# Optimization experiments

Measured on AMD Instinct MI355X. Metric: run time of the kernel, lower is better.

The kernel has to match this reference:

```python
import jax, jax.numpy as jnp
import numpy as np

N_NODES = 50000
N_EDGES = 800000
D_IN = 512
D_OUT = 256


def setup_inputs() -> dict:
    key = jax.random.key(0)
    k1, k2, k3 = jax.random.split(key, 3)
    x = jax.random.normal(k1, (N_NODES, D_IN), dtype=jnp.float32)
    edge_index = jax.random.randint(k2, (2, N_EDGES), 0, N_NODES, dtype=jnp.int64)
    # Glorot-style init for the GCN weight, zero bias (PyG defaults)
    W = jax.random.normal(k3, (D_IN, D_OUT), dtype=jnp.float32) * (1.0 / np.sqrt(D_IN))
    b = jnp.zeros((D_OUT,), dtype=jnp.float32)
    return {"x": x, "edge_index": edge_index, "W": W, "b": b}


def reference(x, edge_index, W, b):
    N = x.shape[0]
    # 1) dense linear transform (the compute-heavy GEMM)
    xw = x @ W  # [N, d_out]

    # 2) add self-loops (PyG GCNConv default)
    loop = jnp.arange(N, dtype=edge_index.dtype)
    row = jnp.concatenate([edge_index[0], loop])  # sources
    col = jnp.concatenate([edge_index[1], loop])  # targets

    # 3) symmetric normalization deg^{-1/2} on targets (in-degree incl. self-loops)
    deg = jax.ops.segment_sum(jnp.ones_like(col, dtype=xw.dtype), col, num_segments=N)
    dinv = jnp.where(deg > 0, jax.lax.rsqrt(deg), 0.0)
    norm = dinv[row] * dinv[col]  # [E+N]

    # 4) gather source features, scale, scatter-add to targets
    msgs = xw[row] * norm[:, None]  # [E+N, d_out]
    agg = jax.ops.segment_sum(msgs, col, num_segments=N)  # [N, d_out]

    # 5) bias + ReLU (dropout is identity in eval mode)
    return jax.nn.relu(agg + b)
```

## Files before the change

kernel.cpp:

```cpp
#include <hip/hip_runtime.h>
#include <hip/hip_bf16.h>

#define N_NODES 50000
#define N_EDGES 800000
#define D_IN    512
#define D_OUT   256
#define NBLK_SCAN ((N_NODES + 1023) / 1024)
#define GEMM_NWG (((N_NODES + 127) / 128) * 2)
#define GEMM_Q   (GEMM_NWG / 8)
#define GEMM_R   (GEMM_NWG % 8)

typedef short s8v  __attribute__((ext_vector_type(8)));
typedef float f32x4 __attribute__((ext_vector_type(4)));

__device__ __forceinline__ unsigned short bf16b(float f) {
    __hip_bfloat16 h = __float2bfloat16(f);
    return *reinterpret_cast<unsigned short*>(&h);
}
__device__ __forceinline__ float bflo(unsigned u) { return __uint_as_float(u << 16); }
__device__ __forceinline__ float bfhi(unsigned u) { return __uint_as_float(u & 0xffff0000u); }

#define GLD16(gp, lp)                                                           \
    __builtin_amdgcn_global_load_lds(                                           \
        (const __attribute__((address_space(1))) unsigned int*)(const void*)(gp),\
        (__attribute__((address_space(3))) unsigned int*)(void*)(lp), 16, 0, 0)

__device__ __forceinline__ int wave_incl_scan(int v, int lane) {
    #pragma unroll
    for (int d = 1; d < 64; d <<= 1) {
        int u = __shfl_up(v, d, 64);
        if (lane >= d) v += u;
    }
    return v;
}


__global__ void k_count(const int* __restrict__ col, int* __restrict__ cnt) {
    int i = (blockIdx.x * 256 + threadIdx.x) * 2;
    if (i < N_EDGES) {
        int2 c = *(const int2*)&col[i];
        atomicAdd(&cnt[c.x], 1);
        atomicAdd(&cnt[c.y], 1);
    }
}

__launch_bounds__(256)
__global__ void k_scan1(const int* __restrict__ cnt, int* __restrict__ bsum) {
    const int t = threadIdx.x, b = blockIdx.x;
    const int idx = b * 1024 + t * 4;
    int4 v = make_int4(0, 0, 0, 0);
    if (idx < N_NODES) v = *(const int4*)&cnt[idx];
    int s = v.x + v.y + v.z + v.w;
    #pragma unroll
    for (int d = 1; d < 64; d <<= 1) s += __shfl_xor(s, d, 64);
    __shared__ int ws[4];
    if ((t & 63) == 0) ws[t >> 6] = s;
    __syncthreads();
    if (t == 0) bsum[b] = ws[0] + ws[1] + ws[2] + ws[3];
}

__launch_bounds__(256)
__global__ void k_scan3(const int* __restrict__ cnt, const int* __restrict__ bsum,
                        int* __restrict__ row_ptr, float* __restrict__ dinv,
                        int* __restrict__ cursor) {
    const int t = threadIdx.x, b = blockIdx.x;
    const int lane = t & 63, wv = t >> 6;
    const int idx = b * 1024 + t * 4;
    int4 v = make_int4(0, 0, 0, 0);
    if (idx < N_NODES) v = *(const int4*)&cnt[idx];
    int s = v.x + v.y + v.z + v.w;
    int isc = wave_incl_scan(s, lane);
    __shared__ int wsum[4];
    __shared__ int s_boff;
    if (lane == 63) wsum[wv] = isc;
    if (t < 64) {
        int u = (t < b) ? bsum[t] : 0;
        #pragma unroll
        for (int d = 1; d < 64; d <<= 1) u += __shfl_xor(u, d, 64);
        if (t == 0) s_boff = u;
    }
    __syncthreads();
    int off = s_boff;
    #pragma unroll
    for (int i = 0; i < 4; ++i)
        if (i < wv) off += wsum[i];
    int p0 = off + isc - s;
    int p1 = p0 + v.x;
    int p2 = p1 + v.y;
    int p3 = p2 + v.z;
    if (idx < N_NODES) {
        row_ptr[idx + 0] = p0; cursor[idx + 0] = p0; dinv[idx + 0] = rsqrtf(1.f + (float)v.x);
        row_ptr[idx + 1] = p1; cursor[idx + 1] = p1; dinv[idx + 1] = rsqrtf(1.f + (float)v.y);
        row_ptr[idx + 2] = p2; cursor[idx + 2] = p2; dinv[idx + 2] = rsqrtf(1.f + (float)v.z);
        row_ptr[idx + 3] = p3; cursor[idx + 3] = p3; dinv[idx + 3] = rsqrtf(1.f + (float)v.w);
    }
    if (b == 0 && t == 0) row_ptr[N_NODES] = N_EDGES;
}

__global__ void k_fill(const int* __restrict__ row, const int* __restrict__ col,
                       int* __restrict__ cursor, int* __restrict__ csr_src) {
    int i = (blockIdx.x * 256 + threadIdx.x) * 2;
    if (i < N_EDGES) {
        int2 c = *(const int2*)&col[i];
        int2 r = *(const int2*)&row[i];
        int p0 = atomicAdd(&cursor[c.x], 1);
        csr_src[p0] = r.x;
        int p1 = atomicAdd(&cursor[c.y], 1);
        csr_src[p1] = r.y;
    }
}

__global__ void k_wt(const float* __restrict__ W, unsigned short* __restrict__ Wt) {
    int k = blockIdx.x;
    int n = threadIdx.x;
    Wt[(size_t)n * D_IN + k] = bf16b(W[(size_t)k * D_OUT + n]);
}

__launch_bounds__(256)
__global__ void k_gemm(const float* __restrict__ A,
                       const unsigned short* __restrict__ Wt,
                       const float* __restrict__ dinv,
                       unsigned short* __restrict__ yb)
{
    __shared__ __align__(16) float          As[128 * 32];
    __shared__ __align__(16) unsigned short Bs[128 * 32];

    int orig = blockIdx.x;
    int xcd = orig % 8, pos = orig / 8;
    int wg = (xcd < GEMM_R) ? xcd * (GEMM_Q + 1) + pos
                            : GEMM_R * (GEMM_Q + 1) + (xcd - GEMM_R) * GEMM_Q + pos;
    const int nt = wg & 1;
    const int mt = wg >> 1;
    const int m0 = mt * 128;
    const int n0 = nt * 128;

    const int t  = threadIdx.x;
    const int w  = t >> 6;
    const int l  = t & 63;
    const int wm = (w >> 1) * 64;
    const int wn = (w & 1) * 64;
    const int lr = l & 15;
    const int lk = l >> 4;

    size_t aoff[4];
    #pragma unroll
    for (int i = 0; i < 4; ++i) {
        int r = m0 + w * 32 + i * 8 + (l >> 3);
        if (r >= N_NODES) r = 0;
        aoff[i] = (size_t)r * D_IN + ((l & 7) ^ (l >> 3)) * 4;
    }
    size_t boff[2];
    #pragma unroll
    for (int i = 0; i < 2; ++i) {
        int r = n0 + w * 32 + i * 16 + (l >> 2);
        boff[i] = (size_t)r * D_IN + ((l & 3) ^ ((l >> 3) & 3)) * 8;
    }

    f32x4 acc[4][4] = {};

    #pragma unroll 1
    for (int tk = 0; tk < 16; ++tk) {
        const int kk = tk * 32;
        {
            char* ab = (char*)As + w * 4096;
            char* bb = (char*)Bs + w * 2048;
            #pragma unroll
            for (int i = 0; i < 4; ++i) GLD16(&A[aoff[i] + kk], ab + i * 1024);
            #pragma unroll
            for (int i = 0; i < 2; ++i) GLD16(&Wt[boff[i] + kk], bb + i * 1024);
        }
        __syncthreads();
        {
            s8v af[4], bfr[4];
            #pragma unroll
            for (int f = 0; f < 4; ++f) {
                int row = wm + f * 16 + lr;
                int s0  = (2 * lk) ^ (lr & 7);
                const char* pr = (const char*)As + row * 128;
                float4 x0 = *(const float4*)(pr + s0 * 16);
                float4 x1 = *(const float4*)(pr + (s0 ^ 1) * 16);
                union { s8v v; unsigned short h[8]; } u;
                u.h[0] = bf16b(x0.x); u.h[1] = bf16b(x0.y);
                u.h[2] = bf16b(x0.z); u.h[3] = bf16b(x0.w);
                u.h[4] = bf16b(x1.x); u.h[5] = bf16b(x1.y);
                u.h[6] = bf16b(x1.z); u.h[7] = bf16b(x1.w);
                af[f] = u.v;
            }
            #pragma unroll
            for (int f = 0; f < 4; ++f) {
                int row = wn + f * 16 + lr;
                int s   = lk ^ ((lr >> 1) & 3);
                bfr[f] = *(const s8v*)((const char*)Bs + row * 64 + s * 16);
            }
            #pragma unroll
            for (int fm = 0; fm < 4; ++fm)
                #pragma unroll
                for (int fn = 0; fn < 4; ++fn)
                    acc[fm][fn] = __builtin_amdgcn_mfma_f32_16x16x32_bf16(
                        af[fm], bfr[fn], acc[fm][fn], 0, 0, 0);
        }
        __syncthreads();
    }

    #pragma unroll
    for (int fm = 0; fm < 4; ++fm) {
        #pragma unroll
        for (int j = 0; j < 4; ++j) {
            int row = m0 + wm + fm * 16 + lk * 4 + j;
            if (row < N_NODES) {
                float s = dinv[row];
                #pragma unroll
                for (int fn = 0; fn < 4; ++fn) {
                    int col = n0 + wn + fn * 16 + lr;
                    yb[(size_t)row * D_OUT + col] = bf16b(acc[fm][fn][j] * s);
                }
            }
        }
    }
}

__device__ __forceinline__ void add8(float* acc, uint4 q) {
    unsigned x;
    x = q.x; acc[0] += bflo(x); acc[1] += bfhi(x);
    x = q.y; acc[2] += bflo(x); acc[3] += bfhi(x);
    x = q.z; acc[4] += bflo(x); acc[5] += bfhi(x);
    x = q.w; acc[6] += bflo(x); acc[7] += bfhi(x);
}

__launch_bounds__(256)
__global__ void k_gather(const int* __restrict__ row_ptr, const int* __restrict__ csr_src,
                         const unsigned short* __restrict__ yb, const float* __restrict__ dinv,
                         const float* __restrict__ bias, float* __restrict__ out)
{
    const int c  = blockIdx.x * 4 + (threadIdx.x >> 6);
    const int l  = threadIdx.x & 63;
    const int eg = l >> 5;
    const int cs = l & 31;
    const size_t colb = (size_t)cs * 8;

    float acc[8] = {0.f,0.f,0.f,0.f,0.f,0.f,0.f,0.f};

    const int s = row_ptr[c];
    const int e = row_ptr[c + 1];

    int i = s + eg;
    while (i + 14 < e) {
        int r[8];
        #pragma unroll
        for (int u = 0; u < 8; ++u) r[u] = csr_src[i + 2 * u];
        uint4 v[8];
        #pragma unroll
        for (int u = 0; u < 8; ++u) v[u] = *(const uint4*)&yb[(size_t)r[u] * D_OUT + colb];
        #pragma unroll
        for (int u = 0; u < 8; ++u) add8(acc, v[u]);
        i += 16;
    }
    while (i < e) {
        int r[4];
        #pragma unroll
        for (int u = 0; u < 4; ++u) {
            int p = i + 2 * u;
            r[u] = csr_src[p < e ? p : e - 1];
        }
        uint4 v[4];
        #pragma unroll
        for (int u = 0; u < 4; ++u) v[u] = *(const uint4*)&yb[(size_t)r[u] * D_OUT + colb];
        #pragma unroll
        for (int u = 0; u < 4; ++u)
            if (i + 2 * u < e) add8(acc, v[u]);
        i += 8;
    }

    #pragma unroll
    for (int u = 0; u < 8; ++u) acc[u] += __shfl_xor(acc[u], 32, 64);

    uint4 sv = *(const uint4*)&yb[(size_t)c * D_OUT + colb];
    add8(acc, sv);

    if (eg == 0) {
        const float sc = dinv[c];
        float4 b0 = *(const float4*)&bias[colb];
        float4 b1 = *(const float4*)&bias[colb + 4];
        float4 o0, o1;
        o0.x = fmaxf(fmaf(acc[0], sc, b0.x), 0.f);
        o0.y = fmaxf(fmaf(acc[1], sc, b0.y), 0.f);
        o0.z = fmaxf(fmaf(acc[2], sc, b0.z), 0.f);
        o0.w = fmaxf(fmaf(acc[3], sc, b0.w), 0.f);
        o1.x = fmaxf(fmaf(acc[4], sc, b1.x), 0.f);
        o1.y = fmaxf(fmaf(acc[5], sc, b1.y), 0.f);
        o1.z = fmaxf(fmaf(acc[6], sc, b1.z), 0.f);
        o1.w = fmaxf(fmaf(acc[7], sc, b1.w), 0.f);
        float* dst = &out[(size_t)c * D_OUT + colb];
        *(float4*)dst       = o0;
        *(float4*)(dst + 4) = o1;
    }
}

extern "C" void kernel_launch(void* const* d_in, const int* in_sizes, int n_in,
                              void* d_out, int out_size, void* d_ws, size_t ws_size,
                              hipStream_t stream) {
    const float* x   = (const float*)d_in[0];
    const int*   ei  = (const int*)d_in[1];
    const float* W   = (const float*)d_in[2];
    const float* b   = (const float*)d_in[3];
    float*       out = (float*)d_out;

    const int* row = ei;
    const int* col = ei + N_EDGES;

    char* p = (char*)d_ws;
    unsigned short* yb = (unsigned short*)p;  p += (size_t)N_NODES * D_OUT * 2;
    unsigned short* Wt = (unsigned short*)p;  p += (size_t)D_OUT * D_IN * 2;
    int*   csr_src = (int*)p;                 p += (size_t)N_EDGES * 4;
    int*   cnt     = (int*)p;                 p += (size_t)N_NODES * 4;
    int*   row_ptr = (int*)p;                 p += (size_t)(N_NODES + 4) * 4;
    int*   cursor  = (int*)p;                 p += (size_t)N_NODES * 4;
    float* dinv    = (float*)p;               p += (size_t)N_NODES * 4;
    int*   bsum    = (int*)p;                 p += (size_t)NBLK_SCAN * 4;

    hipMemsetAsync(cnt, 0, (size_t)N_NODES * sizeof(int), stream);
    k_count<<<(N_EDGES / 2 + 255) / 256, 256, 0, stream>>>(col, cnt);
    k_scan1<<<NBLK_SCAN, 256, 0, stream>>>(cnt, bsum);
    k_scan3<<<NBLK_SCAN, 256, 0, stream>>>(cnt, bsum, row_ptr, dinv, cursor);
    k_fill <<<(N_EDGES / 2 + 255) / 256, 256, 0, stream>>>(row, col, cursor, csr_src);
    k_wt   <<<D_IN, D_OUT, 0, stream>>>(W, Wt);

    k_gemm<<<GEMM_NWG, 256, 0, stream>>>(x, Wt, dinv, yb);

    k_gather<<<N_NODES / 4, 256, 0, stream>>>(row_ptr, csr_src, yb, dinv, b, out);
}
```

Before: 209.2 us.

## Retile GEMM to single-wave 64x64 blocks with 32x32 MFMA; fold memset into k_wt

The GEMM moves from 256-thread 128x128 workgroups using 16x16x32 MFMAs to single-wave 64x64 workgroups using 32x32x16 bf16 MFMAs. Blocks are remapped to XCDs with a simple strided mapping, and offsets use 32-bit arithmetic. Separately, the hipMemsetAsync of the degree counts is folded into the weight-transpose kernel, which now runs first, saving one launch. Smaller tiles give more workgroups and fewer cross-wave barriers, but each tile gets less operand reuse and A is re-read four times across the N tiles.

After: 217.0 us. 1.04x slower.

```diff
diff --git a/kernel.cpp b/kernel.cpp
--- a/kernel.cpp
+++ b/kernel.cpp
@@ -6,12 +6,11 @@
 #define D_IN    512
 #define D_OUT   256
 #define NBLK_SCAN ((N_NODES + 1023) / 1024)
-#define GEMM_NWG (((N_NODES + 127) / 128) * 2)
-#define GEMM_Q   (GEMM_NWG / 8)
-#define GEMM_R   (GEMM_NWG % 8)
-
-typedef short s8v  __attribute__((ext_vector_type(8)));
-typedef float f32x4 __attribute__((ext_vector_type(4)));
+#define GEMM_NWG (((N_NODES + 63) / 64) * 4)
+#define GEMM_CPX (GEMM_NWG / 8)
+
+typedef short s8v   __attribute__((ext_vector_type(8)));
+typedef float f32x16 __attribute__((ext_vector_type(16)));
 
 __device__ __forceinline__ unsigned short bf16b(float f) {
     __hip_bfloat16 h = __float2bfloat16(f);
@@ -32,6 +31,15 @@
         if (lane >= d) v += u;
     }
     return v;
+}
+
+__global__ void k_wt(const float* __restrict__ W, unsigned short* __restrict__ Wt,
+                     int* __restrict__ cnt) {
+    int k = blockIdx.x;
+    int n = threadIdx.x;
+    Wt[(size_t)n * D_IN + k] = bf16b(W[(size_t)k * D_OUT + n]);
+    int t = blockIdx.x * 256 + threadIdx.x;
+    if (t < N_NODES) cnt[t] = 0;
 }
 
 
@@ -110,109 +118,101 @@
     }
 }
 
-__global__ void k_wt(const float* __restrict__ W, unsigned short* __restrict__ Wt) {
-    int k = blockIdx.x;
-    int n = threadIdx.x;
-    Wt[(size_t)n * D_IN + k] = bf16b(W[(size_t)k * D_OUT + n]);
-}
-
-__launch_bounds__(256)
+__launch_bounds__(64, 3)
 __global__ void k_gemm(const float* __restrict__ A,
                        const unsigned short* __restrict__ Wt,
                        const float* __restrict__ dinv,
                        unsigned short* __restrict__ yb)
 {
-    __shared__ __align__(16) float          As[128 * 32];
-    __shared__ __align__(16) unsigned short Bs[128 * 32];
+    __shared__ __align__(16) float          As[64 * 32];
+    __shared__ __align__(16) unsigned short Bs[64 * 32];
 
     int orig = blockIdx.x;
-    int xcd = orig % 8, pos = orig / 8;
-    int wg = (xcd < GEMM_R) ? xcd * (GEMM_Q + 1) + pos
-                            : GEMM_R * (GEMM_Q + 1) + (xcd - GEMM_R) * GEMM_Q + pos;
-    const int nt = wg & 1;
-    const int mt = wg >> 1;
-    const int m0 = mt * 128;
-    const int n0 = nt * 128;
-
-    const int t  = threadIdx.x;
-    const int w  = t >> 6;
-    const int l  = t & 63;
-    const int wm = (w >> 1) * 64;
-    const int wn = (w & 1) * 64;
-    const int lr = l & 15;
-    const int lk = l >> 4;
-
-    size_t aoff[4];
+    int wg = (orig & 7) * GEMM_CPX + (orig >> 3);
+    const int mt = wg >> 2;
+    const int nt = wg & 3;
+    const int m0 = mt * 64;
+    const int n0 = nt * 64;
+
+    const int l  = threadIdx.x;
+    const int l5 = l >> 5;
+    const int lc = l & 31;
+
+    unsigned aoff[8];
+    #pragma unroll
+    for (int i = 0; i < 8; ++i) {
+        int r = m0 + i * 8 + (l >> 3);
+        if (r >= N_NODES) r = 0;
+        aoff[i] = (unsigned)r * D_IN + ((l & 7) ^ (l >> 3)) * 4;
+    }
+    unsigned boff[4];
     #pragma unroll
     for (int i = 0; i < 4; ++i) {
-        int r = m0 + w * 32 + i * 8 + (l >> 3);
-        if (r >= N_NODES) r = 0;
-        aoff[i] = (size_t)r * D_IN + ((l & 7) ^ (l >> 3)) * 4;
-    }
-    size_t boff[2];
-    #pragma unroll
-    for (int i = 0; i < 2; ++i) {
-        int r = n0 + w * 32 + i * 16 + (l >> 2);
-        boff[i] = (size_t)r * D_IN + ((l & 3) ^ ((l >> 3) & 3)) * 8;
-    }
-
-    f32x4 acc[4][4] = {};
+        int c = n0 + i * 16 + (l >> 2);
+        boff[i] = (unsigned)c * D_IN + ((l & 3) ^ ((l >> 3) & 3)) * 8;
+    }
+
+    f32x16 acc[2][2] = {};
 
     #pragma unroll 1
     for (int tk = 0; tk < 16; ++tk) {
         const int kk = tk * 32;
-        {
-            char* ab = (char*)As + w * 4096;
-            char* bb = (char*)Bs + w * 2048;
+        #pragma unroll
+        for (int i = 0; i < 8; ++i) GLD16(&A[aoff[i] + kk], (char*)As + i * 1024);
+        #pragma unroll
+        for (int i = 0; i < 4; ++i) GLD16(&Wt[boff[i] + kk], (char*)Bs + i * 1024);
+        __syncthreads();
+
+        s8v af[2][2], bf[2][2];
+        #pragma unroll
+        for (int rb = 0; rb < 2; ++rb) {
             #pragma unroll
-            for (int i = 0; i < 4; ++i) GLD16(&A[aoff[i] + kk], ab + i * 1024);
-            #pragma unroll
-            for (int i = 0; i < 2; ++i) GLD16(&Wt[boff[i] + kk], bb + i * 1024);
-        }
-        __syncthreads();
-        {
-            s8v af[4], bfr[4];
-            #pragma unroll
-            for (int f = 0; f < 4; ++f) {
-                int row = wm + f * 16 + lr;
-                int s0  = (2 * lk) ^ (lr & 7);
+            for (int k16 = 0; k16 < 2; ++k16) {
+                int row  = rb * 32 + lc;
+                int slog = 4 * k16 + 2 * l5;
                 const char* pr = (const char*)As + row * 128;
-                float4 x0 = *(const float4*)(pr + s0 * 16);
-                float4 x1 = *(const float4*)(pr + (s0 ^ 1) * 16);
+                float4 x0 = *(const float4*)(pr + ((slog    ) ^ (row & 7)) * 16);
+                float4 x1 = *(const float4*)(pr + ((slog + 1) ^ (row & 7)) * 16);
                 union { s8v v; unsigned short h[8]; } u;
                 u.h[0] = bf16b(x0.x); u.h[1] = bf16b(x0.y);
                 u.h[2] = bf16b(x0.z); u.h[3] = bf16b(x0.w);
                 u.h[4] = bf16b(x1.x); u.h[5] = bf16b(x1.y);
                 u.h[6] = bf16b(x1.z); u.h[7] = bf16b(x1.w);
-                af[f] = u.v;
+                af[rb][k16] = u.v;
             }
+        }
+        #pragma unroll
+        for (int cb = 0; cb < 2; ++cb) {
             #pragma unroll
-            for (int f = 0; f < 4; ++f) {
-                int row = wn + f * 16 + lr;
-                int s   = lk ^ ((lr >> 1) & 3);
-                bfr[f] = *(const s8v*)((const char*)Bs + row * 64 + s * 16);
+            for (int k16 = 0; k16 < 2; ++k16) {
+                int row  = cb * 32 + lc;
+                int slog = 2 * k16 + l5;
+                int s    = slog ^ ((row >> 1) & 3);
+                bf[cb][k16] = *(const s8v*)((const char*)Bs + row * 64 + s * 16);
             }
+        }
+        #pragma unroll
+        for (int rb = 0; rb < 2; ++rb)
             #pragma unroll
-            for (int fm = 0; fm < 4; ++fm)
+            for (int cb = 0; cb < 2; ++cb)
                 #pragma unroll
-                for (int fn = 0; fn < 4; ++fn)
-                    acc[fm][fn] = __builtin_amdgcn_mfma_f32_16x16x32_bf16(
-                        af[fm], bfr[fn], acc[fm][fn], 0, 0, 0);
-        }
+                for (int k16 = 0; k16 < 2; ++k16)
+                    acc[rb][cb] = __builtin_amdgcn_mfma_f32_32x32x16_bf16(
+                        af[rb][k16], bf[cb][k16], acc[rb][cb], 0, 0, 0);
         __syncthreads();
     }
 
     #pragma unroll
-    for (int fm = 0; fm < 4; ++fm) {
-        #pragma unroll
-        for (int j = 0; j < 4; ++j) {
-            int row = m0 + wm + fm * 16 + lk * 4 + j;
-            if (row < N_NODES) {
-                float s = dinv[row];
-                #pragma unroll
-                for (int fn = 0; fn < 4; ++fn) {
-                    int col = n0 + wn + fn * 16 + lr;
-                    yb[(size_t)row * D_OUT + col] = bf16b(acc[fm][fn][j] * s);
+    for (int rb = 0; rb < 2; ++rb) {
+        #pragma unroll
+        for (int cb = 0; cb < 2; ++cb) {
+            #pragma unroll
+            for (int j = 0; j < 16; ++j) {
+                int ri  = (j & 3) + 8 * (j >> 2) + 4 * l5;
+                int row = m0 + rb * 32 + ri;
+                if (row < N_NODES) {
+                    int col = n0 + cb * 32 + lc;
+                    yb[(size_t)row * D_OUT + col] = bf16b(acc[rb][cb][j] * dinv[row]);
                 }
             }
         }
@@ -318,14 +318,13 @@
     float* dinv    = (float*)p;               p += (size_t)N_NODES * 4;
     int*   bsum    = (int*)p;                 p += (size_t)NBLK_SCAN * 4;
 
-    hipMemsetAsync(cnt, 0, (size_t)N_NODES * sizeof(int), stream);
+    k_wt   <<<D_IN, D_OUT, 0, stream>>>(W, Wt, cnt);
     k_count<<<(N_EDGES / 2 + 255) / 256, 256, 0, stream>>>(col, cnt);
     k_scan1<<<NBLK_SCAN, 256, 0, stream>>>(cnt, bsum);
     k_scan3<<<NBLK_SCAN, 256, 0, stream>>>(cnt, bsum, row_ptr, dinv, cursor);
     k_fill <<<(N_EDGES / 2 + 255) / 256, 256, 0, stream>>>(row, col, cursor, csr_src);
-    k_wt   <<<D_IN, D_OUT, 0, stream>>>(W, Wt);
-
-    k_gemm<<<GEMM_NWG, 256, 0, stream>>>(x, Wt, dinv, yb);
+
+    k_gemm<<<GEMM_NWG, 64, 0, stream>>>(x, Wt, dinv, yb);
 
     k_gather<<<N_NODES / 4, 256, 0, stream>>>(row_ptr, csr_src, yb, dinv, b, out);
 }
```

## Load GEMM operands directly from global into registers and fold memset into k_wt

Applied to the files above, without the earlier changes.

The GEMM drops the LDS staging path (global_load_lds plus barriers) and has each lane load its A and B fragments straight from global memory into registers before the MFMAs, with a partially unrolled k loop. The counter zeroing that used a separate memset is moved into the weight-transpose kernel, which now runs first, removing one launch. Without LDS the A rows are fetched redundantly by both N-tile waves and loads are less coalesced, so it relies on L2/L1 hits, and global latency is no longer hidden behind a shared tile.

Measured after the change: 258.1 us. 1.23x slower.

```diff
diff --git a/kernel.cpp b/kernel.cpp
--- a/kernel.cpp
+++ b/kernel.cpp
@@ -10,7 +10,7 @@
 #define GEMM_Q   (GEMM_NWG / 8)
 #define GEMM_R   (GEMM_NWG % 8)
 
-typedef short s8v  __attribute__((ext_vector_type(8)));
+typedef short s8v   __attribute__((ext_vector_type(8)));
 typedef float f32x4 __attribute__((ext_vector_type(4)));
 
 __device__ __forceinline__ unsigned short bf16b(float f) {
@@ -20,11 +20,6 @@
 __device__ __forceinline__ float bflo(unsigned u) { return __uint_as_float(u << 16); }
 __device__ __forceinline__ float bfhi(unsigned u) { return __uint_as_float(u & 0xffff0000u); }
 
-#define GLD16(gp, lp)                                                           \
-    __builtin_amdgcn_global_load_lds(                                           \
-        (const __attribute__((address_space(1))) unsigned int*)(const void*)(gp),\
-        (__attribute__((address_space(3))) unsigned int*)(void*)(lp), 16, 0, 0)
-
 __device__ __forceinline__ int wave_incl_scan(int v, int lane) {
     #pragma unroll
     for (int d = 1; d < 64; d <<= 1) {
@@ -32,6 +27,15 @@
         if (lane >= d) v += u;
     }
     return v;
+}
+
+__global__ void k_wt(const float* __restrict__ W, unsigned short* __restrict__ Wt,
+                     int* __restrict__ cnt) {
+    int k = blockIdx.x;
+    int n = threadIdx.x;
+    Wt[(size_t)n * D_IN + k] = bf16b(W[(size_t)k * D_OUT + n]);
+    int t = blockIdx.x * 256 + threadIdx.x;
+    if (t < N_NODES) cnt[t] = 0;
 }
 
 
@@ -110,21 +114,12 @@
     }
 }
 
-__global__ void k_wt(const float* __restrict__ W, unsigned short* __restrict__ Wt) {
-    int k = blockIdx.x;
-    int n = threadIdx.x;
-    Wt[(size_t)n * D_IN + k] = bf16b(W[(size_t)k * D_OUT + n]);
-}
-
 __launch_bounds__(256)
 __global__ void k_gemm(const float* __restrict__ A,
                        const unsigned short* __restrict__ Wt,
                        const float* __restrict__ dinv,
                        unsigned short* __restrict__ yb)
 {
-    __shared__ __align__(16) float          As[128 * 32];
-    __shared__ __align__(16) unsigned short Bs[128 * 32];
-
     int orig = blockIdx.x;
     int xcd = orig % 8, pos = orig / 8;
     int wg = (xcd < GEMM_R) ? xcd * (GEMM_Q + 1) + pos
@@ -142,64 +137,49 @@
     const int lr = l & 15;
     const int lk = l >> 4;
 
-    size_t aoff[4];
-    #pragma unroll
-    for (int i = 0; i < 4; ++i) {
-        int r = m0 + w * 32 + i * 8 + (l >> 3);
+    const float* arow[4];
+    const unsigned short* brow[4];
+    #pragma unroll
+    for (int f = 0; f < 4; ++f) {
+        int r = m0 + wm + f * 16 + lr;
         if (r >= N_NODES) r = 0;
-        aoff[i] = (size_t)r * D_IN + ((l & 7) ^ (l >> 3)) * 4;
-    }
-    size_t boff[2];
-    #pragma unroll
-    for (int i = 0; i < 2; ++i) {
-        int r = n0 + w * 32 + i * 16 + (l >> 2);
-        boff[i] = (size_t)r * D_IN + ((l & 3) ^ ((l >> 3) & 3)) * 8;
+        arow[f] = A  + (size_t)r * D_IN + lk * 8;
+        int c = n0 + wn + f * 16 + lr;
+        brow[f] = Wt + (size_t)c * D_IN + lk * 8;
     }
 
     f32x4 acc[4][4] = {};
 
-    #pragma unroll 1
-    for (int tk = 0; tk < 16; ++tk) {
-        const int kk = tk * 32;
-        {
-            char* ab = (char*)As + w * 4096;
-            char* bb = (char*)Bs + w * 2048;
+    #pragma unroll 4
+    for (int kk = 0; kk < D_IN; kk += 32) {
+        float4 a0[4], a1[4];
+        uint4  bq[4];
+        #pragma unroll
+        for (int f = 0; f < 4; ++f) {
+            a0[f] = *(const float4*)(arow[f] + kk);
+            a1[f] = *(const float4*)(arow[f] + kk + 4);
+        }
+        #pragma unroll
+        for (int f = 0; f < 4; ++f)
+            bq[f] = *(const uint4*)(brow[f] + kk);
+
+        s8v af[4], bf[4];
+        #pragma unroll
+        for (int f = 0; f < 4; ++f) {
+            union { s8v v; unsigned short h[8]; } u;
+            u.h[0] = bf16b(a0[f].x); u.h[1] = bf16b(a0[f].y);
+            u.h[2] = bf16b(a0[f].z); u.h[3] = bf16b(a0[f].w);
+            u.h[4] = bf16b(a1[f].x); u.h[5] = bf16b(a1[f].y);
+            u.h[6] = bf16b(a1[f].z); u.h[7] = bf16b(a1[f].w);
+            af[f] = u.v;
+            bf[f] = *(const s8v*)&bq[f];
+        }
+        #pragma unroll
+        for (int fm = 0; fm < 4; ++fm)
             #pragma unroll
-            for (int i = 0; i < 4; ++i) GLD16(&A[aoff[i] + kk], ab + i * 1024);
-            #pragma unroll
-            for (int i = 0; i < 2; ++i) GLD16(&Wt[boff[i] + kk], bb + i * 1024);
-        }
-        __syncthreads();
-        {
-            s8v af[4], bfr[4];
-            #pragma unroll
-            for (int f = 0; f < 4; ++f) {
-                int row = wm + f * 16 + lr;
-                int s0  = (2 * lk) ^ (lr & 7);
-                const char* pr = (const char*)As + row * 128;
-                float4 x0 = *(const float4*)(pr + s0 * 16);
-                float4 x1 = *(const float4*)(pr + (s0 ^ 1) * 16);
-                union { s8v v; unsigned short h[8]; } u;
-                u.h[0] = bf16b(x0.x); u.h[1] = bf16b(x0.y);
-                u.h[2] = bf16b(x0.z); u.h[3] = bf16b(x0.w);
-                u.h[4] = bf16b(x1.x); u.h[5] = bf16b(x1.y);
-                u.h[6] = bf16b(x1.z); u.h[7] = bf16b(x1.w);
-                af[f] = u.v;
-            }
-            #pragma unroll
-            for (int f = 0; f < 4; ++f) {
-                int row = wn + f * 16 + lr;
-                int s   = lk ^ ((lr >> 1) & 3);
-                bfr[f] = *(const s8v*)((const char*)Bs + row * 64 + s * 16);
-            }
-            #pragma unroll
-            for (int fm = 0; fm < 4; ++fm)
-                #pragma unroll
-                for (int fn = 0; fn < 4; ++fn)
-                    acc[fm][fn] = __builtin_amdgcn_mfma_f32_16x16x32_bf16(
-                        af[fm], bfr[fn], acc[fm][fn], 0, 0, 0);
-        }
-        __syncthreads();
+            for (int fn = 0; fn < 4; ++fn)
+                acc[fm][fn] = __builtin_amdgcn_mfma_f32_16x16x32_bf16(
+                    af[fm], bf[fn], acc[fm][fn], 0, 0, 0);
     }
 
     #pragma unroll
@@ -318,12 +298,11 @@
     float* dinv    = (float*)p;               p += (size_t)N_NODES * 4;
     int*   bsum    = (int*)p;                 p += (size_t)NBLK_SCAN * 4;
 
-    hipMemsetAsync(cnt, 0, (size_t)N_NODES * sizeof(int), stream);
+    k_wt   <<<D_IN, D_OUT, 0, stream>>>(W, Wt, cnt);
     k_count<<<(N_EDGES / 2 + 255) / 256, 256, 0, stream>>>(col, cnt);
     k_scan1<<<NBLK_SCAN, 256, 0, stream>>>(cnt, bsum);
     k_scan3<<<NBLK_SCAN, 256, 0, stream>>>(cnt, bsum, row_ptr, dinv, cursor);
     k_fill <<<(N_EDGES / 2 + 255) / 256, 256, 0, stream>>>(row, col, cursor, csr_src);
-    k_wt   <<<D_IN, D_OUT, 0, stream>>>(W, Wt);
 
     k_gemm<<<GEMM_NWG, 256, 0, stream>>>(x, Wt, dinv, yb);
 
```
